# Kernel optimization log

Measured on AMD Instinct MI355X. Metric: run time of the kernel, lower is better.

Reference implementation:

```python
import jax, jax.numpy as jnp
import numpy as np


def squash(s, axis=-1):
    sq = jnp.sum(s * s, axis=axis, keepdims=True)
    return sq / (1.0 + sq) * s / (jnp.sqrt(sq) + 1e-8)


def setup_inputs() -> dict:
    key = jax.random.key(0)
    k1, k2 = jax.random.split(key)
    B, IN_CAPS, IN_DIM = 32, 2048, 16
    NUM_CAPS, CAPS_DIM = 32, 32
    x = jax.random.normal(k1, (B, IN_CAPS, IN_DIM), dtype=jnp.float32)
    W = 0.01 * jax.random.normal(k2, (NUM_CAPS, IN_CAPS, CAPS_DIM, IN_DIM), dtype=jnp.float32)
    return {"x": x, "W": W, "routing_steps": 3}


def reference(x, W, routing_steps):
    # u_hat[b, j, i, c] = W[j, i, c, d] @ x[b, i, d]
    u_hat = jnp.einsum('jicd,bid->bjic', W, x)
    du = jax.lax.stop_gradient(u_hat)  # routing uses detached predictions
    B, J, I, C = u_hat.shape
    b = jnp.zeros((B, J, I, 1), dtype=u_hat.dtype)
    for _ in range(routing_steps - 1):
        c = jax.nn.softmax(b, axis=1)                  # over output capsules j
        s = jnp.sum(c * du, axis=2)                    # [B, J, C]
        v = squash(s)
        b = b + jnp.einsum('bjic,bjc->bji', du, v)[..., None]
    c = jax.nn.softmax(b, axis=1)
    s = jnp.sum(c * u_hat, axis=2)
    v = squash(s)                                      # [B, J, C]
    return v
```

## Files before the change

kernel.cpp:

```cpp
#include <hip/hip_runtime.h>
#include <hip/hip_bf16.h>

#define B_SZ   32
#define I_CAPS 2048
#define J_CAPS 32
#define C_DIM  32
#define D_DIM  16

#define IT     8
#define TILES  8
#define SPLIT  32
#define ROW_STRIDE 40

typedef _Float16 f16x8 __attribute__((ext_vector_type(8)));
typedef float    f32x4 __attribute__((ext_vector_type(4)));

__device__ inline unsigned short f2bf(float f) {
    union { __hip_bfloat16 h; unsigned short u; } cv;
    cv.h = __float2bfloat16(f);
    return cv.u;
}
__device__ inline float bf2f(unsigned int u16) {
    unsigned int x = (u16 & 0xffffu) << 16;
    union { unsigned int u; float f; } cv; cv.u = x;
    return cv.f;
}

#define MPAD 72

__global__ __launch_bounds__(256) void uhat_mfma(const float* __restrict__ W,
                                                 const float* __restrict__ x,
                                                 unsigned short* __restrict__ u) {
    const int t    = threadIdx.x;
    const int wave = t >> 6;
    const int lane = t & 63;
    const int lm   = lane & 15;
    const int lq   = lane >> 4;

    __shared__ unsigned short tr[4][32 * MPAD];
    unsigned short* my = tr[wave];

    const int i = blockIdx.x;

    f16x8 bfr[2];
#pragma unroll
    for (int nt = 0; nt < 2; ++nt) {
        const int b = nt * 16 + lm;
        const float4 xv = *reinterpret_cast<const float4*>(
            &x[((size_t)b * I_CAPS + i) * D_DIM + lq * 4]);
        f16x8 f = {};
        f[0] = (_Float16)xv.x; f[1] = (_Float16)xv.y;
        f[2] = (_Float16)xv.z; f[3] = (_Float16)xv.w;
        bfr[nt] = f;
    }

    float4 wv[16];
#pragma unroll
    for (int k = 0; k < 16; ++k) {
        const int mt = wave * 16 + k;
        const int j  = mt >> 1;
        const int c  = (mt & 1) * 16 + lm;
        wv[k] = *reinterpret_cast<const float4*>(
            &W[(((size_t)j * I_CAPS + i) * C_DIM + c) * D_DIM + lq * 4]);
    }

#pragma unroll
    for (int g = 0; g < 4; ++g) {
#pragma unroll
        for (int k4 = 0; k4 < 4; ++k4) {
            const int k = g * 4 + k4;
            f16x8 a = {};
            a[0] = (_Float16)wv[k].x; a[1] = (_Float16)wv[k].y;
            a[2] = (_Float16)wv[k].z; a[3] = (_Float16)wv[k].w;

            const f32x4 z = {0.f, 0.f, 0.f, 0.f};
            f32x4 d0 = __builtin_amdgcn_mfma_f32_16x16x32_f16(a, bfr[0], z, 0, 0, 0);
            f32x4 d1 = __builtin_amdgcn_mfma_f32_16x16x32_f16(a, bfr[1], z, 0, 0, 0);

            const int m_loc = k4 * 16 + lq * 4;
#pragma unroll
            for (int nt = 0; nt < 2; ++nt) {
                const f32x4 d = nt ? d1 : d0;
                ushort4 o;
                o.x = f2bf(d[0]); o.y = f2bf(d[1]); o.z = f2bf(d[2]); o.w = f2bf(d[3]);
                const int b = nt * 16 + lm;
                *reinterpret_cast<ushort4*>(&my[b * MPAD + m_loc]) = o;
            }
        }
        asm volatile("s_waitcnt lgkmcnt(0)" ::: "memory");
        __builtin_amdgcn_sched_barrier(0);

        const int b_off = lane >> 3;
        const int m_off = (lane & 7) * 8;
        const int m_base = wave * 256 + g * 64;
#pragma unroll
        for (int gb = 0; gb < 4; ++gb) {
            const int b = gb * 8 + b_off;
            const uint4 v = *reinterpret_cast<const uint4*>(&my[b * MPAD + m_off]);
            *reinterpret_cast<uint4*>(
                &u[((size_t)b * I_CAPS + i) * (J_CAPS * C_DIM) + m_base + m_off]) = v;
        }
    }
}

__global__ __launch_bounds__(256) void route_kernel(const unsigned short* __restrict__ u,
                                                    const float* __restrict__ V,
                                                    float* __restrict__ s) {
    const int b      = blockIdx.y;
    const int i_base = blockIdx.x * (IT * TILES);
    const int t      = threadIdx.x;

    __shared__ unsigned short us[IT * J_CAPS * ROW_STRIDE];
    __shared__ float Vs[J_CAPS * 33];
    __shared__ float cjs[IT * J_CAPS];

    for (int n = t; n < J_CAPS * C_DIM; n += 256) {
        const int j = n >> 5, c = n & 31;
        Vs[j * 33 + c] = V[((size_t)b * J_CAPS + j) * C_DIM + c];
    }

    const int jA = t & 31, iA = t >> 5;
    const int jB = t >> 3, c4 = (t & 7) * 4;

    float sacc0 = 0.f, sacc1 = 0.f, sacc2 = 0.f, sacc3 = 0.f;

    for (int tile = 0; tile < TILES; ++tile) {
        const int i0 = i_base + tile * IT;
        __syncthreads();

        {
            const uint4* gsrc = reinterpret_cast<const uint4*>(
                u + ((size_t)b * I_CAPS + i0) * J_CAPS * C_DIM);
#pragma unroll
            for (int k = 0; k < 4; ++k) {
                const int n  = t + k * 256;
                const int il = n >> 7, rem = n & 127, j = rem >> 2, q = rem & 3;
                *reinterpret_cast<uint4*>(
                    &us[(il * J_CAPS + j) * ROW_STRIDE + q * 8]) = gsrc[n];
            }
        }
        __syncthreads();

        {
            const unsigned short* row = &us[(iA * J_CAPS + jA) * ROW_STRIDE];
            float l = 0.f;
#pragma unroll
            for (int cq = 0; cq < 8; ++cq) {
                const uint2 pk = *reinterpret_cast<const uint2*>(row + cq * 4);
                const float* Vr = &Vs[jA * 33 + cq * 4];
                l += bf2f(pk.x) * Vr[0] + bf2f(pk.x >> 16) * Vr[1]
                   + bf2f(pk.y) * Vr[2] + bf2f(pk.y >> 16) * Vr[3];
            }
            float m = l;
#pragma unroll
            for (int msk = 16; msk >= 1; msk >>= 1) m = fmaxf(m, __shfl_xor(m, msk));
            const float e = __expf(l - m);
            float ssum = e;
#pragma unroll
            for (int msk = 16; msk >= 1; msk >>= 1) ssum += __shfl_xor(ssum, msk);
            cjs[iA * J_CAPS + jA] = e / ssum;
        }
        __syncthreads();

        {
#pragma unroll
            for (int il = 0; il < IT; ++il) {
                const float cj = cjs[il * J_CAPS + jB];
                const unsigned short* row = &us[(il * J_CAPS + jB) * ROW_STRIDE + c4];
                const uint2 pk = *reinterpret_cast<const uint2*>(row);
                sacc0 += cj * bf2f(pk.x);
                sacc1 += cj * bf2f(pk.x >> 16);
                sacc2 += cj * bf2f(pk.y);
                sacc3 += cj * bf2f(pk.y >> 16);
            }
        }
    }

    float* sp = &s[((size_t)b * J_CAPS + jB) * C_DIM + c4];
    atomicAdd(sp + 0, sacc0);
    atomicAdd(sp + 1, sacc1);
    atomicAdd(sp + 2, sacc2);
    atomicAdd(sp + 3, sacc3);
}

__global__ __launch_bounds__(256) void squash_kernel(float* __restrict__ s,
                                                     float* __restrict__ V,
                                                     float* __restrict__ out,
                                                     int final_pass) {
    const int t   = threadIdx.x;
    const int row = blockIdx.x * 8 + (t >> 5);
    const int c   = t & 31;
    const float sv = s[row * 32 + c];
    float sq = sv * sv;
#pragma unroll
    for (int msk = 16; msk >= 1; msk >>= 1) sq += __shfl_xor(sq, msk);
    const float scale = sq / ((1.f + sq) * (sqrtf(sq) + 1e-8f));
    const float v = sv * scale;
    if (final_pass) out[row * 32 + c] = v;
    else            V[row * 32 + c] += v;
    s[row * 32 + c] = 0.f;
}

extern "C" void kernel_launch(void* const* d_in, const int* in_sizes, int n_in,
                              void* d_out, int out_size, void* d_ws, size_t ws_size,
                              hipStream_t stream) {
    const float* x = (const float*)d_in[0];
    const float* W = (const float*)d_in[1];
    float* out = (float*)d_out;

    unsigned short* u = (unsigned short*)d_ws;
    float* s = (float*)((char*)d_ws + (size_t)B_SZ * I_CAPS * J_CAPS * C_DIM * 2);
    float* V = s + B_SZ * J_CAPS * C_DIM;

    hipMemsetAsync(s, 0, 2 * (size_t)B_SZ * J_CAPS * C_DIM * sizeof(float), stream);

    uhat_mfma<<<I_CAPS, 256, 0, stream>>>(W, x, u);

    for (int p = 0; p < 3; ++p) {
        route_kernel<<<dim3(SPLIT, B_SZ), 256, 0, stream>>>(u, V, s);
        squash_kernel<<<(B_SZ * J_CAPS * C_DIM) / 256, 256, 0, stream>>>(s, V, out, p == 2 ? 1 : 0);
    }
}
```

Measured before the change: 165.6 us.

## Fuse squash into routing passes, skip softmax on first pass, process two capsules per block

The separate squash kernels between routing passes are removed. Each routing pass now recomputes squash of the previous partial sums itself, and the accumulated V is kept in a separate buffer with triple-buffered s arrays. The first pass skips the logit dot product and softmax by using uniform coefficients. Predictions are stored as fp16 instead of bf16, which keeps more mantissa at the cost of range. The u_hat kernel also handles two input capsules per block so loads for both are issued before compute. Together this cuts kernel launches and redundant work, at the price of higher register pressure in uhat_mfma.

Result: slower. 189.1 us (+14.2%).

```diff
diff --git a/kernel.cpp b/kernel.cpp
--- a/kernel.cpp
+++ b/kernel.cpp
@@ -13,20 +13,90 @@
 #define ROW_STRIDE 40
 
 typedef _Float16 f16x8 __attribute__((ext_vector_type(8)));
+typedef _Float16 f16x4 __attribute__((ext_vector_type(4)));
 typedef float    f32x4 __attribute__((ext_vector_type(4)));
 
-__device__ inline unsigned short f2bf(float f) {
-    union { __hip_bfloat16 h; unsigned short u; } cv;
-    cv.h = __float2bfloat16(f);
-    return cv.u;
-}
-__device__ inline float bf2f(unsigned int u16) {
-    unsigned int x = (u16 & 0xffffu) << 16;
-    union { unsigned int u; float f; } cv; cv.u = x;
-    return cv.f;
-}
+__device__ __forceinline__ float h2f_lo(unsigned int p) {
+    union { unsigned short s; _Float16 h; } cv; cv.s = (unsigned short)(p & 0xffffu);
+    return (float)cv.h;
+}
+__device__ __forceinline__ float h2f_hi(unsigned int p) { return h2f_lo(p >> 16); }
 
 #define MPAD 72
+#define IPB  2
+
+__device__ __forceinline__ void load_i(const float* __restrict__ W,
+                                       const float* __restrict__ x,
+                                       int i, int wave, int lm, int lq,
+                                       float4 (&wv)[16], float4 (&xv)[2]) {
+#pragma unroll
+    for (int nt = 0; nt < 2; ++nt) {
+        const int b = nt * 16 + lm;
+        xv[nt] = *reinterpret_cast<const float4*>(
+            &x[((size_t)b * I_CAPS + i) * D_DIM + lq * 4]);
+    }
+#pragma unroll
+    for (int k = 0; k < 16; ++k) {
+        const int mt = wave * 16 + k;
+        const int j  = mt >> 1;
+        const int c  = (mt & 1) * 16 + lm;
+        wv[k] = *reinterpret_cast<const float4*>(
+            &W[(((size_t)j * I_CAPS + i) * C_DIM + c) * D_DIM + lq * 4]);
+    }
+}
+
+__device__ __forceinline__ void compute_i(int i, int wave, int lane, int lm, int lq,
+                                          const float4 (&wv)[16], const float4 (&xv)[2],
+                                          unsigned short* __restrict__ my,
+                                          unsigned short* __restrict__ u) {
+    f16x8 bfr[2];
+#pragma unroll
+    for (int nt = 0; nt < 2; ++nt) {
+        f16x8 f = {};
+        f[0] = (_Float16)xv[nt].x; f[1] = (_Float16)xv[nt].y;
+        f[2] = (_Float16)xv[nt].z; f[3] = (_Float16)xv[nt].w;
+        bfr[nt] = f;
+    }
+
+#pragma unroll
+    for (int g = 0; g < 4; ++g) {
+#pragma unroll
+        for (int k4 = 0; k4 < 4; ++k4) {
+            const int k = g * 4 + k4;
+            f16x8 a = {};
+            a[0] = (_Float16)wv[k].x; a[1] = (_Float16)wv[k].y;
+            a[2] = (_Float16)wv[k].z; a[3] = (_Float16)wv[k].w;
+
+            const f32x4 z = {0.f, 0.f, 0.f, 0.f};
+            f32x4 d0 = __builtin_amdgcn_mfma_f32_16x16x32_f16(a, bfr[0], z, 0, 0, 0);
+            f32x4 d1 = __builtin_amdgcn_mfma_f32_16x16x32_f16(a, bfr[1], z, 0, 0, 0);
+
+            const int m_loc = k4 * 16 + lq * 4;
+#pragma unroll
+            for (int nt = 0; nt < 2; ++nt) {
+                const f32x4 d = nt ? d1 : d0;
+                f16x4 o;
+                o[0] = (_Float16)d[0]; o[1] = (_Float16)d[1];
+                o[2] = (_Float16)d[2]; o[3] = (_Float16)d[3];
+                const int b = nt * 16 + lm;
+                *reinterpret_cast<f16x4*>(&my[b * MPAD + m_loc]) = o;
+            }
+        }
+        asm volatile("s_waitcnt lgkmcnt(0)" ::: "memory");
+        __builtin_amdgcn_sched_barrier(0);
+
+        const int b_off = lane >> 3;
+        const int m_off = (lane & 7) * 8;
+        const int m_base = wave * 256 + g * 64;
+#pragma unroll
+        for (int gb = 0; gb < 4; ++gb) {
+            const int b = gb * 8 + b_off;
+            const uint4 v = *reinterpret_cast<const uint4*>(&my[b * MPAD + m_off]);
+            *reinterpret_cast<uint4*>(
+                &u[((size_t)b * I_CAPS + i) * (J_CAPS * C_DIM) + m_base + m_off]) = v;
+        }
+    }
+}
 
 __global__ __launch_bounds__(256) void uhat_mfma(const float* __restrict__ W,
                                                  const float* __restrict__ x,
@@ -40,87 +110,51 @@
     __shared__ unsigned short tr[4][32 * MPAD];
     unsigned short* my = tr[wave];
 
-    const int i = blockIdx.x;
-
-    f16x8 bfr[2];
-#pragma unroll
-    for (int nt = 0; nt < 2; ++nt) {
-        const int b = nt * 16 + lm;
-        const float4 xv = *reinterpret_cast<const float4*>(
-            &x[((size_t)b * I_CAPS + i) * D_DIM + lq * 4]);
-        f16x8 f = {};
-        f[0] = (_Float16)xv.x; f[1] = (_Float16)xv.y;
-        f[2] = (_Float16)xv.z; f[3] = (_Float16)xv.w;
-        bfr[nt] = f;
-    }
-
-    float4 wv[16];
-#pragma unroll
-    for (int k = 0; k < 16; ++k) {
-        const int mt = wave * 16 + k;
-        const int j  = mt >> 1;
-        const int c  = (mt & 1) * 16 + lm;
-        wv[k] = *reinterpret_cast<const float4*>(
-            &W[(((size_t)j * I_CAPS + i) * C_DIM + c) * D_DIM + lq * 4]);
-    }
-
-#pragma unroll
-    for (int g = 0; g < 4; ++g) {
-#pragma unroll
-        for (int k4 = 0; k4 < 4; ++k4) {
-            const int k = g * 4 + k4;
-            f16x8 a = {};
-            a[0] = (_Float16)wv[k].x; a[1] = (_Float16)wv[k].y;
-            a[2] = (_Float16)wv[k].z; a[3] = (_Float16)wv[k].w;
-
-            const f32x4 z = {0.f, 0.f, 0.f, 0.f};
-            f32x4 d0 = __builtin_amdgcn_mfma_f32_16x16x32_f16(a, bfr[0], z, 0, 0, 0);
-            f32x4 d1 = __builtin_amdgcn_mfma_f32_16x16x32_f16(a, bfr[1], z, 0, 0, 0);
-
-            const int m_loc = k4 * 16 + lq * 4;
-#pragma unroll
-            for (int nt = 0; nt < 2; ++nt) {
-                const f32x4 d = nt ? d1 : d0;
-                ushort4 o;
-                o.x = f2bf(d[0]); o.y = f2bf(d[1]); o.z = f2bf(d[2]); o.w = f2bf(d[3]);
-                const int b = nt * 16 + lm;
-                *reinterpret_cast<ushort4*>(&my[b * MPAD + m_loc]) = o;
-            }
-        }
-        asm volatile("s_waitcnt lgkmcnt(0)" ::: "memory");
-        __builtin_amdgcn_sched_barrier(0);
-
-        const int b_off = lane >> 3;
-        const int m_off = (lane & 7) * 8;
-        const int m_base = wave * 256 + g * 64;
-#pragma unroll
-        for (int gb = 0; gb < 4; ++gb) {
-            const int b = gb * 8 + b_off;
-            const uint4 v = *reinterpret_cast<const uint4*>(&my[b * MPAD + m_off]);
-            *reinterpret_cast<uint4*>(
-                &u[((size_t)b * I_CAPS + i) * (J_CAPS * C_DIM) + m_base + m_off]) = v;
-        }
-    }
-}
-
-__global__ __launch_bounds__(256) void route_kernel(const unsigned short* __restrict__ u,
-                                                    const float* __restrict__ V,
-                                                    float* __restrict__ s) {
+    const int i0 = blockIdx.x * IPB;
+
+    float4 wvA[16], wvB[16], xvA[2], xvB[2];
+    load_i(W, x, i0,     wave, lm, lq, wvA, xvA);
+    load_i(W, x, i0 + 1, wave, lm, lq, wvB, xvB);
+    compute_i(i0,     wave, lane, lm, lq, wvA, xvA, my, u);
+    compute_i(i0 + 1, wave, lane, lm, lq, wvB, xvB, my, u);
+}
+
+__global__ __launch_bounds__(256) void route_pass(const unsigned short* __restrict__ u,
+                                                  const float* __restrict__ s_prev,
+                                                  float* __restrict__ V1,
+                                                  float* __restrict__ s_out,
+                                                  int pass) {
     const int b      = blockIdx.y;
-    const int i_base = blockIdx.x * (IT * TILES);
+    const int isplit = blockIdx.x;
+    const int i_base = isplit * (IT * TILES);
     const int t      = threadIdx.x;
 
     __shared__ unsigned short us[IT * J_CAPS * ROW_STRIDE];
     __shared__ float Vs[J_CAPS * 33];
     __shared__ float cjs[IT * J_CAPS];
 
-    for (int n = t; n < J_CAPS * C_DIM; n += 256) {
-        const int j = n >> 5, c = n & 31;
-        Vs[j * 33 + c] = V[((size_t)b * J_CAPS + j) * C_DIM + c];
-    }
-
     const int jA = t & 31, iA = t >> 5;
     const int jB = t >> 3, c4 = (t & 7) * 4;
+
+    if (pass > 0) {
+        const size_t base = ((size_t)b * J_CAPS + jB) * C_DIM + c4;
+        const float4 sv = *reinterpret_cast<const float4*>(&s_prev[base]);
+        float sq = sv.x * sv.x + sv.y * sv.y + sv.z * sv.z + sv.w * sv.w;
+#pragma unroll
+        for (int msk = 4; msk >= 1; msk >>= 1) sq += __shfl_xor(sq, msk);
+        const float scale = sq / ((1.f + sq) * (sqrtf(sq) + 1e-8f));
+        float4 v;
+        v.x = sv.x * scale; v.y = sv.y * scale;
+        v.z = sv.z * scale; v.w = sv.w * scale;
+        if (pass == 1 && isplit == 0)
+            *reinterpret_cast<float4*>(&V1[base]) = v;
+        if (pass == 2) {
+            const float4 v1 = *reinterpret_cast<const float4*>(&V1[base]);
+            v.x += v1.x; v.y += v1.y; v.z += v1.z; v.w += v1.w;
+        }
+        Vs[jB * 33 + c4 + 0] = v.x; Vs[jB * 33 + c4 + 1] = v.y;
+        Vs[jB * 33 + c4 + 2] = v.z; Vs[jB * 33 + c4 + 3] = v.w;
+    }
 
     float sacc0 = 0.f, sacc1 = 0.f, sacc2 = 0.f, sacc3 = 0.f;
 
@@ -141,15 +175,17 @@
         }
         __syncthreads();
 
-        {
+        if (pass == 0) {
+            cjs[iA * J_CAPS + jA] = 1.0f / 32.0f;
+        } else {
             const unsigned short* row = &us[(iA * J_CAPS + jA) * ROW_STRIDE];
             float l = 0.f;
 #pragma unroll
             for (int cq = 0; cq < 8; ++cq) {
                 const uint2 pk = *reinterpret_cast<const uint2*>(row + cq * 4);
                 const float* Vr = &Vs[jA * 33 + cq * 4];
-                l += bf2f(pk.x) * Vr[0] + bf2f(pk.x >> 16) * Vr[1]
-                   + bf2f(pk.y) * Vr[2] + bf2f(pk.y >> 16) * Vr[3];
+                l += h2f_lo(pk.x) * Vr[0] + h2f_hi(pk.x) * Vr[1]
+                   + h2f_lo(pk.y) * Vr[2] + h2f_hi(pk.y) * Vr[3];
             }
             float m = l;
 #pragma unroll
@@ -168,25 +204,23 @@
                 const float cj = cjs[il * J_CAPS + jB];
                 const unsigned short* row = &us[(il * J_CAPS + jB) * ROW_STRIDE + c4];
                 const uint2 pk = *reinterpret_cast<const uint2*>(row);
-                sacc0 += cj * bf2f(pk.x);
-                sacc1 += cj * bf2f(pk.x >> 16);
-                sacc2 += cj * bf2f(pk.y);
-                sacc3 += cj * bf2f(pk.y >> 16);
-            }
-        }
-    }
-
-    float* sp = &s[((size_t)b * J_CAPS + jB) * C_DIM + c4];
+                sacc0 += cj * h2f_lo(pk.x);
+                sacc1 += cj * h2f_hi(pk.x);
+                sacc2 += cj * h2f_lo(pk.y);
+                sacc3 += cj * h2f_hi(pk.y);
+            }
+        }
+    }
+
+    float* sp = &s_out[((size_t)b * J_CAPS + jB) * C_DIM + c4];
     atomicAdd(sp + 0, sacc0);
     atomicAdd(sp + 1, sacc1);
     atomicAdd(sp + 2, sacc2);
     atomicAdd(sp + 3, sacc3);
 }
 
-__global__ __launch_bounds__(256) void squash_kernel(float* __restrict__ s,
-                                                     float* __restrict__ V,
-                                                     float* __restrict__ out,
-                                                     int final_pass) {
+__global__ __launch_bounds__(256) void squash_out(const float* __restrict__ s,
+                                                  float* __restrict__ out) {
     const int t   = threadIdx.x;
     const int row = blockIdx.x * 8 + (t >> 5);
     const int c   = t & 31;
@@ -195,10 +229,7 @@
 #pragma unroll
     for (int msk = 16; msk >= 1; msk >>= 1) sq += __shfl_xor(sq, msk);
     const float scale = sq / ((1.f + sq) * (sqrtf(sq) + 1e-8f));
-    const float v = sv * scale;
-    if (final_pass) out[row * 32 + c] = v;
-    else            V[row * 32 + c] += v;
-    s[row * 32 + c] = 0.f;
+    out[row * 32 + c] = sv * scale;
 }
 
 extern "C" void kernel_launch(void* const* d_in, const int* in_sizes, int n_in,
@@ -208,16 +239,22 @@
     const float* W = (const float*)d_in[1];
     float* out = (float*)d_out;
 
+    const size_t u_elems = (size_t)B_SZ * I_CAPS * J_CAPS * C_DIM;
+    const size_t sjc     = (size_t)B_SZ * J_CAPS * C_DIM;
+
     unsigned short* u = (unsigned short*)d_ws;
-    float* s = (float*)((char*)d_ws + (size_t)B_SZ * I_CAPS * J_CAPS * C_DIM * 2);
-    float* V = s + B_SZ * J_CAPS * C_DIM;
-
-    hipMemsetAsync(s, 0, 2 * (size_t)B_SZ * J_CAPS * C_DIM * sizeof(float), stream);
-
-    uhat_mfma<<<I_CAPS, 256, 0, stream>>>(W, x, u);
-
-    for (int p = 0; p < 3; ++p) {
-        route_kernel<<<dim3(SPLIT, B_SZ), 256, 0, stream>>>(u, V, s);
-        squash_kernel<<<(B_SZ * J_CAPS * C_DIM) / 256, 256, 0, stream>>>(s, V, out, p == 2 ? 1 : 0);
-    }
-}
+    float* s0 = (float*)((char*)d_ws + u_elems * 2);
+    float* s1 = s0 + sjc;
+    float* s2 = s1 + sjc;
+    float* V1 = s2 + sjc;
+
+    hipMemsetAsync(s0, 0, 4 * sjc * sizeof(float), stream);
+
+    uhat_mfma<<<I_CAPS / IPB, 256, 0, stream>>>(W, x, u);
+
+    route_pass<<<dim3(SPLIT, B_SZ), 256, 0, stream>>>(u, nullptr, V1, s0, 0);
+    route_pass<<<dim3(SPLIT, B_SZ), 256, 0, stream>>>(u, s0, V1, s1, 1);
+    route_pass<<<dim3(SPLIT, B_SZ), 256, 0, stream>>>(u, s1, V1, s2, 2);
+
+    squash_out<<<(B_SZ * J_CAPS * C_DIM) / 256, 256, 0, stream>>>(s2, out);
+}
```
